# Kernel optimization log

Hardware: AMD Instinct MI355X
Metric: run time of the kernel (lower is better)

Reference implementation:

```python
import jax, jax.numpy as jnp
import numpy as np

N_VERTS = 6890
N_JOINTS = 24
SMPL_PARENT = np.array([0, 0, 0, 1, 2, 3, 4, 5, 6, 7, 8, 9, 9, 9, 12, 13, 14, 16, 17, 18, 19, 20, 21], dtype=np.int32)  # parent of joints 1..23


def rodrigues(r):
    """Axis-angle [N,3] -> rotation matrices [N,3,3]."""
    eps = 1e-8
    theta = jnp.linalg.norm(r, axis=-1, keepdims=True) + eps  # [N,1]
    a = r / theta                                             # unit axis [N,3]
    c = jnp.cos(theta)[..., None]                             # [N,1,1]
    s = jnp.sin(theta)[..., None]
    ax, ay, az = a[:, 0], a[:, 1], a[:, 2]
    zero = jnp.zeros_like(ax)
    K = jnp.stack([zero, -az, ay,
                   az, zero, -ax,
                   -ay, ax, zero], axis=-1).reshape(-1, 3, 3)  # skew [N,3,3]
    outer = a[:, :, None] * a[:, None, :]                      # [N,3,3]
    I = jnp.eye(3, dtype=r.dtype)
    return c * I + (1.0 - c) * outer + s * K


def setup_inputs() -> dict:
    key = jax.random.key(0)
    ks = jax.random.split(key, 7)
    B = 512
    pose = jax.random.normal(ks[0], (B, 72), dtype=jnp.float32) * 0.3
    beta = jax.random.normal(ks[1], (B, 10), dtype=jnp.float32)
    v_template = jax.random.normal(ks[2], (N_VERTS, 3), dtype=jnp.float32)
    shapedirs = jax.random.normal(ks[3], (N_VERTS, 3, 10), dtype=jnp.float32) * 0.01
    posedirs = jax.random.normal(ks[4], (N_VERTS, 3, 207), dtype=jnp.float32) * 0.01
    J_regressor = jax.random.uniform(ks[5], (N_JOINTS, N_VERTS), dtype=jnp.float32)
    J_regressor = J_regressor / jnp.sum(J_regressor, axis=1, keepdims=True)
    weights = jax.random.uniform(ks[6], (N_VERTS, N_JOINTS), dtype=jnp.float32)
    weights = weights / jnp.sum(weights, axis=1, keepdims=True)
    parent = jnp.asarray(SMPL_PARENT)
    return {"pose": pose, "beta": beta, "v_template": v_template,
            "shapedirs": shapedirs, "posedirs": posedirs,
            "J_regressor": J_regressor, "weights": weights, "parent": parent}


def smpl_forward(pose, beta, v_template, shapedirs, posedirs, J_regressor, weights, parent):
    B = pose.shape[0]
    dt = pose.dtype
    # shape blendshapes: [6890,3,10] x [B,10] -> [B,6890,3]
    v_shaped = jnp.einsum('vct,bt->bvc', shapedirs, beta) + v_template[None]
    # rest joints: [24,6890] x [B,6890,3] -> [B,24,3]
    J = jnp.einsum('jv,bvc->bjc', J_regressor, v_shaped)
    # axis-angle -> rotmats
    R = rodrigues(pose.reshape(-1, 3)).reshape(B, N_JOINTS, 3, 3)
    # pose blendshapes from non-root rotations minus identity
    lrotmin = (R[:, 1:] - jnp.eye(3, dtype=dt)).reshape(B, 207)
    v_posed = v_shaped + jnp.einsum('vcp,bp->bvc', posedirs, lrotmin)
    # relative joint offsets
    J_rel = jnp.concatenate([J[:, :1], J[:, 1:] - J[:, parent]], axis=1)  # [B,24,3]
    # local 4x4 transforms
    G_local = jnp.concatenate([R, J_rel[:, :, :, None]], axis=-1)        # [B,24,3,4]
    pad_row = jnp.broadcast_to(jnp.array([0., 0., 0., 1.], dtype=dt).reshape(1, 1, 1, 4),
                               (B, N_JOINTS, 1, 4))
    G_local = jnp.concatenate([G_local, pad_row], axis=2)                # [B,24,4,4]
    # accumulate along kinematic chain (fixed 24-joint unrolled loop)
    Gs = [G_local[:, 0]]
    for i in range(1, N_JOINTS):
        Gs.append(jnp.matmul(Gs[int(SMPL_PARENT[i - 1])], G_local[:, i]))
    G = jnp.stack(Gs, axis=1)                                            # [B,24,4,4]
    # subtract rest-pose contribution (only affects last column)
    rest_vec = jnp.concatenate([J, jnp.zeros((B, N_JOINTS, 1), dtype=dt)], axis=2)  # [B,24,4]
    rest = jnp.zeros((B, N_JOINTS, 4, 4), dtype=dt).at[:, :, :, 3].set(
        jnp.einsum('bjxy,bjy->bjx', G, rest_vec))
    G = G - rest
    # linear blend skinning: [6890,24] x [B,24,4,4] -> [B,6890,4,4]
    T = jnp.einsum('vj,bjxy->bvxy', weights, G)
    rest_shape_h = jnp.concatenate([v_posed, jnp.ones((B, N_VERTS, 1), dtype=dt)], axis=-1)
    v = jnp.einsum('bvxy,bvy->bvx', T, rest_shape_h)[:, :, :3]
    return v


def reference(pose, beta, v_template, shapedirs, posedirs, J_regressor, weights, parent):
    return smpl_forward(pose, beta, v_template, shapedirs, posedirs, J_regressor, weights, parent)
```

## Files before the change

### kernel.cpp

```cpp
#include <hip/hip_runtime.h>

#define NV 6890
#define NVP16 6912
#define NJ 24
#define BATCH 512
#define NCOL 20670
#define NCOLP 20736
#define KK 224
#define JCH 864
#define PSTR 104
#define MTB 32

typedef float f4 __attribute__((ext_vector_type(4)));
typedef float f32x4 __attribute__((ext_vector_type(4)));
typedef float f32x16 __attribute__((ext_vector_type(16)));
typedef short bf16x8 __attribute__((ext_vector_type(8)));
typedef unsigned short ushort8 __attribute__((ext_vector_type(8)));


__device__ __forceinline__ unsigned short bf16_rne(float x) {
  union { float f; unsigned u; } c; c.f = x;
  unsigned r = c.u + 0x7fffu + ((c.u >> 16) & 1u);
  return (unsigned short)(r >> 16);
}
__device__ __forceinline__ float bf16lo_f(unsigned u) {
  union { unsigned u; float f; } c; c.u = u << 16; return c.f;
}
__device__ __forceinline__ float bf16hi_f(unsigned u) {
  union { unsigned u; float f; } c; c.u = u & 0xFFFF0000u; return c.f;
}

__global__ void k_pre(const float* __restrict__ Jreg, const float* __restrict__ vtemp,
                      const float* __restrict__ sdirs, const float* __restrict__ pdirs,
                      const float* __restrict__ wgt,
                      float* __restrict__ partial, unsigned short* __restrict__ Bbuf,
                      unsigned short* __restrict__ Wb2) {
  int bid = blockIdx.x;
  int tid = threadIdx.x;
  if (bid < 192) {
    int j = bid >> 3, bz = bid & 7;
    float acc[33];
#pragma unroll
    for (int i = 0; i < 33; ++i) acc[i] = 0.f;
    int v0 = bz * JCH;
    int v1 = v0 + JCH; if (v1 > NV) v1 = NV;
    for (int v = v0 + tid; v < v1; v += 256) {
      float w = Jreg[(size_t)j * NV + v];
      const float* vt = vtemp + (size_t)v * 3;
      acc[0] += w * vt[0]; acc[1] += w * vt[1]; acc[2] += w * vt[2];
      const float* sdv = sdirs + (size_t)v * 30;
#pragma unroll
      for (int t = 0; t < 30; ++t) acc[3 + t] += w * sdv[t];
    }
#pragma unroll
    for (int i = 0; i < 33; ++i) {
      float a = acc[i];
#pragma unroll
      for (int s = 32; s > 0; s >>= 1) a += __shfl_xor(a, s, 64);
      acc[i] = a;
    }
    __shared__ float red[4][34];
    int lane = tid & 63, wv = tid >> 6;
    if (lane == 0) {
#pragma unroll
      for (int i = 0; i < 33; ++i) red[wv][i] = acc[i];
    }
    __syncthreads();
    if (tid < 33) {
      float s = red[0][tid] + red[1][tid] + red[2][tid] + red[3][tid];
      partial[((size_t)j * 8 + bz) * 33 + tid] = s;
    }
    return;
  }
  int idx = (bid - 192) * 256 + tid;
  if (idx < NCOLP * 28) {
    int n = idx / 28, k8 = idx % 28;
    int kc = k8 >> 2, h = k8 & 3;
    ushort8 o;
#pragma unroll
    for (int e = 0; e < 8; ++e) {
      int k = k8 * 8 + e;
      float v = 0.f;
      if (n < NCOL) {
        if (k < 207) v = pdirs[(size_t)n * 207 + k];
        else if (k < 217) v = sdirs[(size_t)n * 10 + (k - 207)];
      }
      o[e] = bf16_rne(v);
    }
    size_t dst = ((size_t)(n >> 4) * 7 + kc) * 512 + (size_t)(h * 16 + (n & 15)) * 8;
    *(ushort8*)(Bbuf + dst) = o;
  } else {
    int widx = idx - NCOLP * 28;
    int v = widx >> 2, q = widx & 3;
    ushort8 o = {0, 0, 0, 0, 0, 0, 0, 0};
    if (v < NV && q < 3) {
#pragma unroll
      for (int e = 0; e < 8; ++e) o[e] = bf16_rne(wgt[(size_t)v * 24 + q * 8 + e]);
    }
    int km = q >> 1;
    int lhalf = q & 1;
    size_t dst = ((size_t)(v >> 5) * 2 + km) * 512 + (size_t)((v & 31) + 32 * lhalf) * 8;
    *(ushort8*)(Wb2 + dst) = o;
  }
}

__global__ void k_batch(const float* __restrict__ pose, const float* __restrict__ beta,
                        const int* __restrict__ parent, const float* __restrict__ partial,
                        unsigned short* __restrict__ Abuf, unsigned short* __restrict__ Amd2) {
  int tid = threadIdx.x;
  int g = tid >> 6;
  int j = tid & 63;
  int b = blockIdx.x * 4 + g;
  __shared__ float JS[NJ][33];
  __shared__ float jl[4][NJ][3];
  __shared__ float gl[4][NJ][16];

  {
    ushort8 z = {0, 0, 0, 0, 0, 0, 0, 0};
    *(ushort8*)(Amd2 + (size_t)blockIdx.x * 2048 + tid * 8) = z;
  }

  for (int i = tid; i < NJ * 33; i += 256) {
    int jj = i / 33, q = i % 33;
    float s = 0.f;
#pragma unroll
    for (int bz = 0; bz < 8; ++bz) s += partial[((size_t)jj * 8 + bz) * 33 + q];
    JS[jj][q] = s;
  }
  __syncthreads();

  float bt[10];
#pragma unroll
  for (int t = 0; t < 10; ++t) bt[t] = beta[b * 10 + t];

  float R[9];
  float Jj[3] = {0.f, 0.f, 0.f};
  if (j < NJ) {
#pragma unroll
    for (int c = 0; c < 3; ++c) {
      float a = JS[j][c];
#pragma unroll
      for (int t = 0; t < 10; ++t) a += JS[j][3 + c * 10 + t] * bt[t];
      Jj[c] = a;
      jl[g][j][c] = a;
    }
    float rx = pose[b * 72 + j * 3 + 0];
    float ry = pose[b * 72 + j * 3 + 1];
    float rz = pose[b * 72 + j * 3 + 2];
    float theta = sqrtf(rx * rx + ry * ry + rz * rz) + 1e-8f;
    float inv = 1.f / theta;
    float ax = rx * inv, ay = ry * inv, az = rz * inv;
    float c = cosf(theta), s = sinf(theta), oc = 1.f - c;
    R[0] = c + oc * ax * ax;      R[1] = oc * ax * ay - s * az; R[2] = oc * ax * az + s * ay;
    R[3] = oc * ax * ay + s * az; R[4] = c + oc * ay * ay;      R[5] = oc * ay * az - s * ax;
    R[6] = oc * ax * az - s * ay; R[7] = oc * ay * az + s * ax; R[8] = c + oc * az * az;
  }
  __syncthreads();

  if (j >= 1 && j < NJ) {
    unsigned short* lr = Abuf + b * KK + (j - 1) * 9;
#pragma unroll
    for (int k = 0; k < 9; ++k)
      lr[k] = bf16_rne(R[k] - ((k == 0 || k == 4 || k == 8) ? 1.f : 0.f));
  }
  if (j >= 32 && j < 42) Abuf[b * KK + 207 + (j - 32)] = bf16_rne(bt[j - 32]);
  if (j >= 42 && j < 49) Abuf[b * KK + 207 + (j - 32)] = 0;

  if (j < NJ) {
    int par = (j == 0) ? 0 : parent[j - 1];
#pragma unroll
    for (int r = 0; r < 3; ++r) {
      gl[g][j][r * 4 + 0] = R[r * 3 + 0];
      gl[g][j][r * 4 + 1] = R[r * 3 + 1];
      gl[g][j][r * 4 + 2] = R[r * 3 + 2];
      gl[g][j][r * 4 + 3] = (j == 0) ? Jj[r] : Jj[r] - jl[g][par][r];
    }
  }
  __syncthreads();

  if (j < NJ) {
    int a[12];
    int n = 0, cur = j;
    while (cur != 0 && n < 12) { a[n++] = cur; cur = parent[cur - 1]; }
    float G[12];
#pragma unroll
    for (int r = 0; r < 3; ++r)
#pragma unroll
      for (int cc = 0; cc < 4; ++cc) G[r * 4 + cc] = gl[g][0][r * 4 + cc];
    for (int i = n - 1; i >= 0; --i) {
      const float* L = gl[g][a[i]];
      float C[12];
#pragma unroll
      for (int r = 0; r < 3; ++r) {
#pragma unroll
        for (int cc = 0; cc < 4; ++cc) {
          float sacc = (cc == 3) ? G[r * 4 + 3] : 0.f;
#pragma unroll
          for (int k = 0; k < 3; ++k) sacc += G[r * 4 + k] * L[k * 4 + cc];
          C[r * 4 + cc] = sacc;
        }
      }
#pragma unroll
      for (int k = 0; k < 12; ++k) G[k] = C[k];
    }
    float Aval[12];
#pragma unroll
    for (int r = 0; r < 3; ++r) {
      Aval[r * 4 + 0] = G[r * 4 + 0];
      Aval[r * 4 + 1] = G[r * 4 + 1];
      Aval[r * 4 + 2] = G[r * 4 + 2];
      Aval[r * 4 + 3] = G[r * 4 + 3] -
                        (G[r * 4 + 0] * jl[g][j][0] + G[r * 4 + 1] * jl[g][j][1] +
                         G[r * 4 + 2] * jl[g][j][2]);
    }
    int pair = b >> 1, odd = b & 1;
    int km = j >> 4, kl = j & 15;
    int lhalf = kl >> 3, e = kl & 7;
    unsigned short* base = Amd2 + ((size_t)pair * 2 + km) * 512;
#pragma unroll
    for (int r = 0; r < 3; ++r)
#pragma unroll
      for (int cc = 0; cc < 4; ++cc) {
        int row = odd * 16 + r * 4 + cc;
        base[(row + 32 * lhalf) * 8 + e] = bf16_rne(Aval[r * 4 + cc]);
      }
  }
}

__launch_bounds__(128, 4)
__global__ void k_gemmskin(const unsigned short* __restrict__ Abuf,
                           const unsigned short* __restrict__ Bbuf,
                           const float* __restrict__ vtemp,
                           const unsigned short* __restrict__ Amd2,
                           const unsigned short* __restrict__ Wb2,
                           float* __restrict__ out) {
  __shared__ unsigned vp[2 * 16 * PSTR];

  int bid = blockIdx.x;
  int lin = (bid & 7) * 216 + (bid >> 3);
  int bx = lin >> 4;
  int by = lin & 15;

  int tid = threadIdx.x;
  int w = tid >> 6, lane = tid & 63;
  int lo = lane & 15, hi = lane >> 4;
  int bb0 = by * MTB;
  unsigned* wvp = vp + w * 16 * PSTR;

  bf16x8 Af[2][7];
#pragma unroll
  for (int mt = 0; mt < 2; ++mt) {
    const unsigned short* arow = Abuf + (size_t)(bb0 + mt * 16 + lo) * KK + hi * 8;
#pragma unroll
    for (int kc = 0; kc < 7; ++kc)
      Af[mt][kc] = *(const bf16x8*)(arow + kc * 32);
  }

#pragma unroll
  for (int s = 0; s < 6; ++s) {
    const unsigned short* btile = Bbuf + ((size_t)(bx * 12 + w * 6 + s) * 7) * 512 + lane * 8;
    bf16x8 Bf[7];
#pragma unroll
    for (int kc = 0; kc < 7; ++kc) Bf[kc] = *(const bf16x8*)(btile + kc * 512);
    int gc = bx * 192 + w * 96 + s * 16 + lo;
    float vt = (gc < NCOL) ? vtemp[gc] : 0.f;
#pragma unroll
    for (int mt = 0; mt < 2; ++mt) {
      f32x4 acc = {vt, vt, vt, vt};
#pragma unroll
      for (int kc = 0; kc < 7; ++kc)
        acc = __builtin_amdgcn_mfma_f32_16x16x32_bf16(Af[mt][kc], Bf[kc], acc, 0, 0, 0);
#pragma unroll
      for (int rp = 0; rp < 2; ++rp) {
        unsigned pr = (unsigned)bf16_rne(acc[2 * rp]) |
                      ((unsigned)bf16_rne(acc[2 * rp + 1]) << 16);
        wvp[(mt * 8 + hi * 2 + rp) * PSTR + s * 16 + lo] = pr;
      }
    }
  }

  int v = lane & 31, h32 = lane >> 5;
  int vg = bx * 64 + w * 32 + v;
  bool sok = vg < NV;
  int vt32 = bx * 2 + w;
  bf16x8 Wf0 = *(const bf16x8*)(Wb2 + ((size_t)vt32 * 2 + 0) * 512 + lane * 8);
  bf16x8 Wf1 = *(const bf16x8*)(Wb2 + ((size_t)vt32 * 2 + 1) * 512 + lane * 8);

  int gp0 = by * 16;
  bf16x8 A0c = *(const bf16x8*)(Amd2 + ((size_t)gp0 * 2 + 0) * 512 + lane * 8);
  bf16x8 A1c = *(const bf16x8*)(Amd2 + ((size_t)gp0 * 2 + 1) * 512 + lane * 8);

#pragma unroll 4
  for (int p = 0; p < 16; ++p) {
    bf16x8 A0n, A1n;
    if (p < 15) {
      size_t t = ((size_t)(gp0 + p + 1)) * 2;
      A0n = *(const bf16x8*)(Amd2 + t * 512 + lane * 8);
      A1n = *(const bf16x8*)(Amd2 + (t + 1) * 512 + lane * 8);
    }
    unsigned ux = wvp[p * PSTR + 3 * v + 0];
    unsigned uy = wvp[p * PSTR + 3 * v + 1];
    unsigned uz = wvp[p * PSTR + 3 * v + 2];

    f32x16 acc = {0.f, 0.f, 0.f, 0.f, 0.f, 0.f, 0.f, 0.f,
                  0.f, 0.f, 0.f, 0.f, 0.f, 0.f, 0.f, 0.f};
    acc = __builtin_amdgcn_mfma_f32_32x32x16_bf16(A0c, Wf0, acc, 0, 0, 0);
    acc = __builtin_amdgcn_mfma_f32_32x32x16_bf16(A1c, Wf1, acc, 0, 0, 0);

    float xe = bf16lo_f(ux), ye = bf16lo_f(uy), ze = bf16lo_f(uz);
    float xo = bf16hi_f(ux), yo = bf16hi_f(uy), zo = bf16hi_f(uz);
    float oA = acc[0] * xe + acc[1] * ye + acc[2] * ze + acc[3];
    float oB = acc[4] * xe + acc[5] * ye + acc[6] * ze + acc[7];
    float oC = acc[8] * xo + acc[9] * yo + acc[10] * zo + acc[11];
    float oD = acc[12] * xo + acc[13] * yo + acc[14] * zo + acc[15];

    if (sok) {
      size_t be = (size_t)(bb0 + 2 * p) * NV + vg;
      size_t bo = be + NV;
      out[be * 3 + h32] = oA;
      out[bo * 3 + h32] = oC;
      if (h32 == 0) {
        out[be * 3 + 2] = oB;
        out[bo * 3 + 2] = oD;
      }
    }
    A0c = A0n; A1c = A1n;
  }
}

extern "C" void kernel_launch(void* const* d_in, const int* in_sizes, int n_in,
                              void* d_out, int out_size, void* d_ws, size_t ws_size,
                              hipStream_t stream) {
  const float* pose   = (const float*)d_in[0];
  const float* beta   = (const float*)d_in[1];
  const float* vtemp  = (const float*)d_in[2];
  const float* sdirs  = (const float*)d_in[3];
  const float* pdirs  = (const float*)d_in[4];
  const float* Jreg   = (const float*)d_in[5];
  const float* wgt    = (const float*)d_in[6];
  const int*   parent = (const int*)d_in[7];
  float* out = (float*)d_out;

  char* wsb = (char*)d_ws;
  unsigned short* Abuf = (unsigned short*)wsb;
  unsigned short* Bbuf = (unsigned short*)(wsb + 229376);
  unsigned short* Amd2 = (unsigned short*)(wsb + 9519104);
  float* part          = (float*)(wsb + 10043392);
  unsigned short* Wb2  = (unsigned short*)(wsb + 10068736);

  hipLaunchKernelGGL(k_pre, dim3(192 + (NCOLP * 28 + NVP16 * 4) / 256), dim3(256), 0, stream,
                     Jreg, vtemp, sdirs, pdirs, wgt, part, Bbuf, Wb2);
  hipLaunchKernelGGL(k_batch, dim3(BATCH / 4), dim3(256), 0, stream, pose, beta, parent, part,
                     Abuf, Amd2);
  hipLaunchKernelGGL(k_gemmskin, dim3(1728), dim3(128), 0, stream,
                     Abuf, Bbuf, vtemp, Amd2, Wb2, out);
}
```

Baseline: 48.49 us.

## Split joint regression from weight conversion and fuse conversion with batch kernel

The prep work is reorganised. The joint-regressor reduction now runs alone in a small first kernel. The bf16 conversion of posedirs, shapedirs and weights moves into the per-batch rigid-transform kernel as extra blocks, so the two independent jobs run concurrently and the critical path becomes the short reduction followed by the batch work. Output stores in the skinning GEMM also switch to nontemporal stores to reduce cache pollution. The launch count stays the same, but block scheduling becomes mixed and shared-memory use in the fused kernel could affect occupancy.

```diff
diff --git a/kernel.cpp b/kernel.cpp
--- a/kernel.cpp
+++ b/kernel.cpp
@@ -30,94 +30,97 @@
   union { unsigned u; float f; } c; c.u = u & 0xFFFF0000u; return c.f;
 }
 
-__global__ void k_pre(const float* __restrict__ Jreg, const float* __restrict__ vtemp,
-                      const float* __restrict__ sdirs, const float* __restrict__ pdirs,
-                      const float* __restrict__ wgt,
-                      float* __restrict__ partial, unsigned short* __restrict__ Bbuf,
-                      unsigned short* __restrict__ Wb2) {
+__global__ void k_jreg(const float* __restrict__ Jreg, const float* __restrict__ vtemp,
+                       const float* __restrict__ sdirs, float* __restrict__ partial) {
   int bid = blockIdx.x;
   int tid = threadIdx.x;
-  if (bid < 192) {
-    int j = bid >> 3, bz = bid & 7;
-    float acc[33];
-#pragma unroll
-    for (int i = 0; i < 33; ++i) acc[i] = 0.f;
-    int v0 = bz * JCH;
-    int v1 = v0 + JCH; if (v1 > NV) v1 = NV;
-    for (int v = v0 + tid; v < v1; v += 256) {
-      float w = Jreg[(size_t)j * NV + v];
-      const float* vt = vtemp + (size_t)v * 3;
-      acc[0] += w * vt[0]; acc[1] += w * vt[1]; acc[2] += w * vt[2];
-      const float* sdv = sdirs + (size_t)v * 30;
-#pragma unroll
-      for (int t = 0; t < 30; ++t) acc[3 + t] += w * sdv[t];
-    }
-#pragma unroll
-    for (int i = 0; i < 33; ++i) {
-      float a = acc[i];
-#pragma unroll
-      for (int s = 32; s > 0; s >>= 1) a += __shfl_xor(a, s, 64);
-      acc[i] = a;
-    }
-    __shared__ float red[4][34];
-    int lane = tid & 63, wv = tid >> 6;
-    if (lane == 0) {
-#pragma unroll
-      for (int i = 0; i < 33; ++i) red[wv][i] = acc[i];
-    }
-    __syncthreads();
-    if (tid < 33) {
-      float s = red[0][tid] + red[1][tid] + red[2][tid] + red[3][tid];
-      partial[((size_t)j * 8 + bz) * 33 + tid] = s;
+  int j = bid >> 3, bz = bid & 7;
+  float acc[33];
+#pragma unroll
+  for (int i = 0; i < 33; ++i) acc[i] = 0.f;
+  int v0 = bz * JCH;
+  int v1 = v0 + JCH; if (v1 > NV) v1 = NV;
+  for (int v = v0 + tid; v < v1; v += 256) {
+    float w = Jreg[(size_t)j * NV + v];
+    const float* vt = vtemp + (size_t)v * 3;
+    acc[0] += w * vt[0]; acc[1] += w * vt[1]; acc[2] += w * vt[2];
+    const float* sdv = sdirs + (size_t)v * 30;
+#pragma unroll
+    for (int t = 0; t < 30; ++t) acc[3 + t] += w * sdv[t];
+  }
+#pragma unroll
+  for (int i = 0; i < 33; ++i) {
+    float a = acc[i];
+#pragma unroll
+    for (int s = 32; s > 0; s >>= 1) a += __shfl_xor(a, s, 64);
+    acc[i] = a;
+  }
+  __shared__ float red[4][34];
+  int lane = tid & 63, wv = tid >> 6;
+  if (lane == 0) {
+#pragma unroll
+    for (int i = 0; i < 33; ++i) red[wv][i] = acc[i];
+  }
+  __syncthreads();
+  if (tid < 33) {
+    float s = red[0][tid] + red[1][tid] + red[2][tid] + red[3][tid];
+    partial[((size_t)j * 8 + bz) * 33 + tid] = s;
+  }
+}
+
+__global__ void k_mid(const float* __restrict__ pose, const float* __restrict__ beta,
+                      const int* __restrict__ parent, const float* __restrict__ partial,
+                      const float* __restrict__ pdirs, const float* __restrict__ sdirs,
+                      const float* __restrict__ wgt,
+                      unsigned short* __restrict__ Abuf, unsigned short* __restrict__ Amd2,
+                      unsigned short* __restrict__ Bbuf, unsigned short* __restrict__ Wb2) {
+  int bid = blockIdx.x;
+  int tid = threadIdx.x;
+
+  if (bid >= 128) {
+    int idx = (bid - 128) * 256 + tid;
+    if (idx < NCOLP * 28) {
+      int n = idx / 28, k8 = idx % 28;
+      int kc = k8 >> 2, h = k8 & 3;
+      ushort8 o;
+#pragma unroll
+      for (int e = 0; e < 8; ++e) {
+        int k = k8 * 8 + e;
+        float v = 0.f;
+        if (n < NCOL) {
+          if (k < 207) v = pdirs[(size_t)n * 207 + k];
+          else if (k < 217) v = sdirs[(size_t)n * 10 + (k - 207)];
+        }
+        o[e] = bf16_rne(v);
+      }
+      size_t dst = ((size_t)(n >> 4) * 7 + kc) * 512 + (size_t)(h * 16 + (n & 15)) * 8;
+      *(ushort8*)(Bbuf + dst) = o;
+    } else {
+      int widx = idx - NCOLP * 28;
+      int v = widx >> 2, q = widx & 3;
+      ushort8 o = {0, 0, 0, 0, 0, 0, 0, 0};
+      if (v < NV && q < 3) {
+#pragma unroll
+        for (int e = 0; e < 8; ++e) o[e] = bf16_rne(wgt[(size_t)v * 24 + q * 8 + e]);
+      }
+      int km = q >> 1;
+      int lhalf = q & 1;
+      size_t dst = ((size_t)(v >> 5) * 2 + km) * 512 + (size_t)((v & 31) + 32 * lhalf) * 8;
+      *(ushort8*)(Wb2 + dst) = o;
     }
     return;
   }
-  int idx = (bid - 192) * 256 + tid;
-  if (idx < NCOLP * 28) {
-    int n = idx / 28, k8 = idx % 28;
-    int kc = k8 >> 2, h = k8 & 3;
-    ushort8 o;
-#pragma unroll
-    for (int e = 0; e < 8; ++e) {
-      int k = k8 * 8 + e;
-      float v = 0.f;
-      if (n < NCOL) {
-        if (k < 207) v = pdirs[(size_t)n * 207 + k];
-        else if (k < 217) v = sdirs[(size_t)n * 10 + (k - 207)];
-      }
-      o[e] = bf16_rne(v);
-    }
-    size_t dst = ((size_t)(n >> 4) * 7 + kc) * 512 + (size_t)(h * 16 + (n & 15)) * 8;
-    *(ushort8*)(Bbuf + dst) = o;
-  } else {
-    int widx = idx - NCOLP * 28;
-    int v = widx >> 2, q = widx & 3;
-    ushort8 o = {0, 0, 0, 0, 0, 0, 0, 0};
-    if (v < NV && q < 3) {
-#pragma unroll
-      for (int e = 0; e < 8; ++e) o[e] = bf16_rne(wgt[(size_t)v * 24 + q * 8 + e]);
-    }
-    int km = q >> 1;
-    int lhalf = q & 1;
-    size_t dst = ((size_t)(v >> 5) * 2 + km) * 512 + (size_t)((v & 31) + 32 * lhalf) * 8;
-    *(ushort8*)(Wb2 + dst) = o;
-  }
-}
-
-__global__ void k_batch(const float* __restrict__ pose, const float* __restrict__ beta,
-                        const int* __restrict__ parent, const float* __restrict__ partial,
-                        unsigned short* __restrict__ Abuf, unsigned short* __restrict__ Amd2) {
-  int tid = threadIdx.x;
+
   int g = tid >> 6;
   int j = tid & 63;
-  int b = blockIdx.x * 4 + g;
+  int b = bid * 4 + g;
   __shared__ float JS[NJ][33];
   __shared__ float jl[4][NJ][3];
   __shared__ float gl[4][NJ][16];
 
   {
     ushort8 z = {0, 0, 0, 0, 0, 0, 0, 0};
-    *(ushort8*)(Amd2 + (size_t)blockIdx.x * 2048 + tid * 8) = z;
+    *(ushort8*)(Amd2 + (size_t)bid * 2048 + tid * 8) = z;
   }
 
   for (int i = tid; i < NJ * 33; i += 256) {
@@ -317,11 +320,11 @@
     if (sok) {
       size_t be = (size_t)(bb0 + 2 * p) * NV + vg;
       size_t bo = be + NV;
-      out[be * 3 + h32] = oA;
-      out[bo * 3 + h32] = oC;
+      __builtin_nontemporal_store(oA, &out[be * 3 + h32]);
+      __builtin_nontemporal_store(oC, &out[bo * 3 + h32]);
       if (h32 == 0) {
-        out[be * 3 + 2] = oB;
-        out[bo * 3 + 2] = oD;
+        __builtin_nontemporal_store(oB, &out[be * 3 + 2]);
+        __builtin_nontemporal_store(oD, &out[bo * 3 + 2]);
       }
     }
     A0c = A0n; A1c = A1n;
@@ -348,10 +351,9 @@
   float* part          = (float*)(wsb + 10043392);
   unsigned short* Wb2  = (unsigned short*)(wsb + 10068736);
 
-  hipLaunchKernelGGL(k_pre, dim3(192 + (NCOLP * 28 + NVP16 * 4) / 256), dim3(256), 0, stream,
-                     Jreg, vtemp, sdirs, pdirs, wgt, part, Bbuf, Wb2);
-  hipLaunchKernelGGL(k_batch, dim3(BATCH / 4), dim3(256), 0, stream, pose, beta, parent, part,
-                     Abuf, Amd2);
+  hipLaunchKernelGGL(k_jreg, dim3(192), dim3(256), 0, stream, Jreg, vtemp, sdirs, part);
+  hipLaunchKernelGGL(k_mid, dim3(128 + (NCOLP * 28 + NVP16 * 4) / 256), dim3(256), 0, stream,
+                     pose, beta, parent, part, pdirs, sdirs, wgt, Abuf, Amd2, Bbuf, Wb2);
   hipLaunchKernelGGL(k_gemmskin, dim3(1728), dim3(128), 0, stream,
                      Abuf, Bbuf, vtemp, Amd2, Wb2, out);
 }
```

Measured after the change: 62.01 us. +27.9%, slower.
